# Kernel tuning notes

Measured on AMD Instinct MI355X. Metric: run time of the kernel, lower is better.

Reference implementation:

```python
import jax, jax.numpy as jnp
import numpy as np

B, D, L, H = 2, 64, 512, 1024  # batch, n_docs (timesteps), tokens per doc, bert hidden


def _ln(x, g, b):
    # torch.nn.LayerNorm over last dim, eps=1e-5
    m = jnp.mean(x, axis=-1, keepdims=True)
    v = jnp.mean((x - m) ** 2, axis=-1, keepdims=True)
    return (x - m) / jnp.sqrt(v + 1e-5) * g + b


def _ht(x):
    # Hardtanh(min=-8, max=8)
    return jnp.clip(x, -8.0, 8.0)


def setup_inputs() -> dict:
    key = jax.random.key(0)
    ks = jax.random.split(key, 12)
    xavier = lambda k, shape: jax.random.normal(k, shape, dtype=jnp.float32) * np.float32(np.sqrt(2.0 / sum(shape)))
    return {
        "trans": jax.random.normal(ks[0], (B, D, L, H), dtype=jnp.float32) * 0.1,  # frozen BERT last_hidden_state
        "document_mask": jax.random.bernoulli(ks[1], 0.9, (B, D)),
        "Wf": xavier(ks[2], (H, H)), "bf": jnp.ones((H,), jnp.float32),
        "Wi": xavier(ks[3], (H, H)), "bi": jnp.zeros((H,), jnp.float32),
        "Wg": xavier(ks[4], (H, H)), "bg": jnp.zeros((H,), jnp.float32),
        "Wo": xavier(ks[5], (H, H)), "bo": jnp.zeros((H,), jnp.float32),
        "Wp": xavier(ks[6], (H, H)), "bp": jnp.zeros((H,), jnp.float32),
        "tF": xavier(ks[7], (L,)), "tI": xavier(ks[8], (L,)), "tO": xavier(ks[9], (L,)),
        "c_gamma": jnp.ones((H,), jnp.float32), "c_beta": jnp.zeros((H,), jnp.float32),
        "h_gamma": jnp.ones((H,), jnp.float32), "h_beta": jnp.zeros((H,), jnp.float32),
    }


def _forward(trans, document_mask, Wf, bf, Wi, bi, Wg, bg, Wo, bo, Wp, bp,
             tF, tI, tO, c_gamma, c_beta, h_gamma, h_beta):
    b, d, l, h = trans.shape
    # docFlat @ transform: contract the token (l) axis -> [b, d, h]
    pF = jnp.einsum('bdlh,l->bdh', trans, tF)
    pI = jnp.einsum('bdlh,l->bdh', trans, tI)
    pO = jnp.einsum('bdlh,l->bdh', trans, tO)

    def step(carry, xs):
        c, hs = carry                      # each [b, h]
        pf, pi, po, m = xs                 # [b, h] x3, [b] bool
        nC = _ln(c, c_gamma, c_beta)
        nH = _ln(hs, h_gamma, h_beta)
        f = jax.nn.sigmoid(_ht(nH @ Wf.T + bf) + pf)
        c2 = c * f
        i = jax.nn.sigmoid(_ht(nH @ Wi.T + bi) + pi)
        g = _ht(jax.nn.gelu(nH @ Wg.T + bg, approximate=False) + pi)
        c2 = c2 + i * g
        o = jax.nn.sigmoid(_ht(nH @ Wo.T + bo) + po)
        h2 = o * _ht(jax.nn.gelu(nC @ Wp.T + bp, approximate=False))
        mm = m[:, None]
        h2 = jnp.where(mm, h2, hs)
        c2 = jnp.where(mm, c2, c)
        c2 = jnp.clip(c2, -10.0, 10.0)
        h2 = jnp.clip(h2, -10.0, 10.0)
        return (c2, h2), None

    init = (jnp.zeros((b, h), trans.dtype), jnp.zeros((b, h), trans.dtype))
    xs = (pF.transpose(1, 0, 2), pI.transpose(1, 0, 2), pO.transpose(1, 0, 2), document_mask.T)
    (c_fin, h_fin), _ = jax.lax.scan(step, init, xs)
    return h_fin  # [b, h] (original returns [b, h, 1])


def reference(trans, document_mask, Wf, bf, Wi, bi, Wg, bg, Wo, bo, Wp, bp,
              tF, tI, tO, c_gamma, c_beta, h_gamma, h_beta):
    return _forward(trans, document_mask, Wf, bf, Wi, bi, Wg, bg, Wo, bo, Wp, bp,
                    tF, tI, tO, c_gamma, c_beta, h_gamma, h_beta)
```

## Files before the change

kernel.cpp:

```cpp
#include <hip/hip_runtime.h>
#include <math.h>


#define NBLK 256

__device__ __forceinline__ float sigf(float x)   { return 1.0f / (1.0f + __expf(-x)); }
__device__ __forceinline__ float geluf(float x)  { return 0.5f * x * (1.0f + erff(x * 0.70710678118654752f)); }
__device__ __forceinline__ float clampf(float x, float lo, float hi) { return fminf(fmaxf(x, lo), hi); }

__device__ __forceinline__ void astf(float* p, float v) {
    __hip_atomic_store(p, v, __ATOMIC_RELAXED, __HIP_MEMORY_SCOPE_AGENT);
}
__device__ __forceinline__ float aldf(const float* p) {
    return __hip_atomic_load(p, __ATOMIC_RELAXED, __HIP_MEMORY_SCOPE_AGENT);
}
__device__ __forceinline__ void astu(unsigned* p, unsigned v) {
    __hip_atomic_store(p, v, __ATOMIC_RELAXED, __HIP_MEMORY_SCOPE_AGENT);
}
__device__ __forceinline__ unsigned aldu(const unsigned* p) {
    return __hip_atomic_load(p, __ATOMIC_RELAXED, __HIP_MEMORY_SCOPE_AGENT);
}

__global__ __launch_bounds__(256, 1) void fused_kernel(
    const float* __restrict__ trans, const int* __restrict__ mask,
    const float* __restrict__ Wf, const float* __restrict__ bf,
    const float* __restrict__ Wi, const float* __restrict__ bi,
    const float* __restrict__ Wg, const float* __restrict__ bg,
    const float* __restrict__ Wo, const float* __restrict__ bo,
    const float* __restrict__ Wp, const float* __restrict__ bp,
    const float* __restrict__ tF, const float* __restrict__ tI, const float* __restrict__ tO,
    const float* __restrict__ c_gamma, const float* __restrict__ c_beta,
    const float* __restrict__ h_gamma, const float* __restrict__ h_beta,
    float* __restrict__ ws, float* __restrict__ out)
{
    const int t    = threadIdx.x;
    const int lane = t & 63;
    const int wv   = t >> 6;
    const int blk  = blockIdx.x;
    const int hrow = (blk << 2) + wv;

    unsigned* flags = (unsigned*)ws;
    unsigned* rel   = flags + 256;
    float* stC = ws + 512;
    float* stH = ws + 4608;
    float* pF  = ws + 8704;
    float* pI  = pF + 131072;
    float* pO  = pI + 131072;

    __shared__ float smem[2][4][1024];

    float4 wfr[4], wir[4], wgr[4], wor[4], wpr[4];
    {
        const float4* rf = (const float4*)(Wf + (size_t)hrow * 1024);
        const float4* ri = (const float4*)(Wi + (size_t)hrow * 1024);
        const float4* rg = (const float4*)(Wg + (size_t)hrow * 1024);
        const float4* ro = (const float4*)(Wo + (size_t)hrow * 1024);
        const float4* rp = (const float4*)(Wp + (size_t)hrow * 1024);
        #pragma unroll
        for (int q = 0; q < 4; ++q) {
            const int k4 = lane + 64 * q;
            wfr[q] = rf[k4]; wir[q] = ri[k4]; wgr[q] = rg[k4];
            wor[q] = ro[k4]; wpr[q] = rp[k4];
        }
    }
    const float bfv = bf[hrow], biv = bi[hrow], bgv = bg[hrow], bov = bo[hrow], bpv = bp[hrow];

    {
        float* sF = &smem[0][0][0];
        float* sI = &smem[0][0][512];
        float* sO = &smem[0][1][0];
        sF[t] = tF[t]; sF[t + 256] = tF[t + 256];
        sI[t] = tI[t]; sI[t + 256] = tI[t + 256];
        sO[t] = tO[t]; sO[t + 256] = tO[t + 256];
        __syncthreads();

        const int bd = blk >> 1;
        const int h0 = (blk & 1) * 512;
        const int s  = t & 127;
        const int g  = t >> 7;
        const float4* tr = (const float4*)trans + (size_t)bd * 512 * 256 + (h0 >> 2) + s;

        float4 aF = make_float4(0.f,0.f,0.f,0.f);
        float4 aI = make_float4(0.f,0.f,0.f,0.f);
        float4 aO = make_float4(0.f,0.f,0.f,0.f);
        #pragma unroll 8
        for (int li = 0; li < 256; ++li) {
            const int l = g + 2 * li;
            float4 v = tr[(size_t)l * 256];
            const float wf = sF[l], wi = sI[l], wo = sO[l];
            aF.x = fmaf(v.x, wf, aF.x); aF.y = fmaf(v.y, wf, aF.y);
            aF.z = fmaf(v.z, wf, aF.z); aF.w = fmaf(v.w, wf, aF.w);
            aI.x = fmaf(v.x, wi, aI.x); aI.y = fmaf(v.y, wi, aI.y);
            aI.z = fmaf(v.z, wi, aI.z); aI.w = fmaf(v.w, wi, aI.w);
            aO.x = fmaf(v.x, wo, aO.x); aO.y = fmaf(v.y, wo, aO.y);
            aO.z = fmaf(v.z, wo, aO.z); aO.w = fmaf(v.w, wo, aO.w);
        }
        float4* cmb = (float4*)&smem[0][2][0];
        if (g == 1) { cmb[s] = aF; cmb[128 + s] = aI; cmb[256 + s] = aO; }
        __syncthreads();
        if (g == 0) {
            const float4 bF = cmb[s], bI = cmb[128 + s], bO = cmb[256 + s];
            aF.x += bF.x; aF.y += bF.y; aF.z += bF.z; aF.w += bF.w;
            aI.x += bI.x; aI.y += bI.y; aI.z += bI.z; aI.w += bI.w;
            aO.x += bO.x; aO.y += bO.y; aO.z += bO.z; aO.w += bO.w;
            const int base = bd * 1024 + h0 + 4 * s;
            astf(&pF[base+0], aF.x); astf(&pF[base+1], aF.y);
            astf(&pF[base+2], aF.z); astf(&pF[base+3], aF.w);
            astf(&pI[base+0], aI.x); astf(&pI[base+1], aI.y);
            astf(&pI[base+2], aI.z); astf(&pI[base+3], aI.w);
            astf(&pO[base+0], aO.x); astf(&pO[base+1], aO.y);
            astf(&pO[base+2], aO.z); astf(&pO[base+3], aO.w);
        }
    }
    __syncthreads();
    if (t == 0) astu(&flags[blk], 1u);

    float sfv, siv, sgv, sov, spv, bfb, bib, bgb, bob, bpb;
    {
        float4 gh4[4], bh4[4], gc4[4], bc4[4];
        const float4* Gh = (const float4*)h_gamma;
        const float4* Bh = (const float4*)h_beta;
        const float4* Gc = (const float4*)c_gamma;
        const float4* Bc = (const float4*)c_beta;
        #pragma unroll
        for (int q = 0; q < 4; ++q) {
            const int k4 = lane + 64 * q;
            gh4[q] = Gh[k4]; bh4[q] = Bh[k4]; gc4[q] = Gc[k4]; bc4[q] = Bc[k4];
        }
        bfb = bib = bgb = bob = bpb = 0.f;
        #pragma unroll
        for (int q = 0; q < 4; ++q) {
            bfb += wfr[q].x*bh4[q].x + wfr[q].y*bh4[q].y + wfr[q].z*bh4[q].z + wfr[q].w*bh4[q].w;
            bib += wir[q].x*bh4[q].x + wir[q].y*bh4[q].y + wir[q].z*bh4[q].z + wir[q].w*bh4[q].w;
            bgb += wgr[q].x*bh4[q].x + wgr[q].y*bh4[q].y + wgr[q].z*bh4[q].z + wgr[q].w*bh4[q].w;
            bob += wor[q].x*bh4[q].x + wor[q].y*bh4[q].y + wor[q].z*bh4[q].z + wor[q].w*bh4[q].w;
            bpb += wpr[q].x*bc4[q].x + wpr[q].y*bc4[q].y + wpr[q].z*bc4[q].z + wpr[q].w*bc4[q].w;
        }
        #pragma unroll
        for (int q = 0; q < 4; ++q) {
            wfr[q].x *= gh4[q].x; wfr[q].y *= gh4[q].y; wfr[q].z *= gh4[q].z; wfr[q].w *= gh4[q].w;
            wir[q].x *= gh4[q].x; wir[q].y *= gh4[q].y; wir[q].z *= gh4[q].z; wir[q].w *= gh4[q].w;
            wgr[q].x *= gh4[q].x; wgr[q].y *= gh4[q].y; wgr[q].z *= gh4[q].z; wgr[q].w *= gh4[q].w;
            wor[q].x *= gh4[q].x; wor[q].y *= gh4[q].y; wor[q].z *= gh4[q].z; wor[q].w *= gh4[q].w;
            wpr[q].x *= gc4[q].x; wpr[q].y *= gc4[q].y; wpr[q].z *= gc4[q].z; wpr[q].w *= gc4[q].w;
        }
        sfv = siv = sgv = sov = spv = 0.f;
        #pragma unroll
        for (int q = 0; q < 4; ++q) {
            sfv += wfr[q].x + wfr[q].y + wfr[q].z + wfr[q].w;
            siv += wir[q].x + wir[q].y + wir[q].z + wir[q].w;
            sgv += wgr[q].x + wgr[q].y + wgr[q].z + wgr[q].w;
            sov += wor[q].x + wor[q].y + wor[q].z + wor[q].w;
            spv += wpr[q].x + wpr[q].y + wpr[q].z + wpr[q].w;
        }
        #pragma unroll
        for (int off = 32; off; off >>= 1) {
            sfv += __shfl_xor(sfv, off); siv += __shfl_xor(siv, off);
            sgv += __shfl_xor(sgv, off); sov += __shfl_xor(sov, off);
            spv += __shfl_xor(spv, off);
            bfb += __shfl_xor(bfb, off); bib += __shfl_xor(bib, off);
            bgb += __shfl_xor(bgb, off); bob += __shfl_xor(bob, off);
            bpb += __shfl_xor(bpb, off);
        }
    }

    if (blk == 0) {
        if (wv == 0) {
            for (;;) {
                const unsigned a0 = aldu(&flags[lane]);
                const unsigned a1 = aldu(&flags[lane + 64]);
                const unsigned a2 = aldu(&flags[lane + 128]);
                const unsigned a3 = aldu(&flags[lane + 192]);
                const int ok = (a0 >= 1u) && (a1 >= 1u) && (a2 >= 1u) && (a3 >= 1u);
                if (__all(ok)) break;
                __builtin_amdgcn_s_sleep(1);
            }
            if (lane < 16) astu(&rel[lane * 16], 1u);
        }
    } else if (t == 0) {
        while (aldu(&rel[(blk & 15) * 16]) < 1u) __builtin_amdgcn_s_sleep(2);
    }
    __syncthreads();

    float c_prev = 0.f, h_prev = 0.f;

    for (int d = 0; d < 64; ++d) {
        const int par = d & 1;
        const float* cc = stC + par * 2048;
        const float* hc = stH + par * 2048;
        float* cn = stC + (par ^ 1) * 2048;
        float* hn = stH + (par ^ 1) * 2048;
        float (*sm)[1024] = smem[par];

        float pfv = 0.f, piv = 0.f, pov = 0.f;
        int mv = 1;
        if (lane < 2) {
            const int pidx = (lane * 64 + d) * 1024 + hrow;
            pfv = aldf(&pF[pidx]); piv = aldf(&pI[pidx]); pov = aldf(&pO[pidx]);
            mv = mask[lane * 64 + d];
        }

        {
            const unsigned tgt = (unsigned)(d + 1);
            if (blk == 0) {
                if (wv == 0) {
                    for (;;) {
                        const unsigned a0 = aldu(&flags[lane]);
                        const unsigned a1 = aldu(&flags[lane + 64]);
                        const unsigned a2 = aldu(&flags[lane + 128]);
                        const unsigned a3 = aldu(&flags[lane + 192]);
                        const int ok = (a0 >= tgt) && (a1 >= tgt) && (a2 >= tgt) && (a3 >= tgt);
                        if (__all(ok)) break;
                        __builtin_amdgcn_s_sleep(1);
                    }
                    if (lane < 16) astu(&rel[lane * 16], tgt);
                }
            } else if (t == 0) {
                while (aldu(&rel[(blk & 15) * 16]) < tgt) __builtin_amdgcn_s_sleep(2);
            }
            __syncthreads();
        }

        float lh0[4], lh1[4], lc0[4], lc1[4];
        #pragma unroll
        for (int j = 0; j < 4; ++j) {
            const int e = t + 256 * j;
            lh0[j] = aldf(hc + e);        lh1[j] = aldf(hc + 1024 + e);
            lc0[j] = aldf(cc + e);        lc1[j] = aldf(cc + 1024 + e);
        }
        #pragma unroll
        for (int j = 0; j < 4; ++j) {
            const int e = t + 256 * j;
            sm[0][e] = lh0[j]; sm[1][e] = lh1[j];
            sm[2][e] = lc0[j]; sm[3][e] = lc1[j];
        }
        __syncthreads();

        float zf0=0,zf1=0,zi0=0,zi1=0,zg0=0,zg1=0,zo0=0,zo1=0,zp0=0,zp1=0;
        float sH0=0,qH0=0,sH1=0,qH1=0,sC0=0,qC0=0,sC1=0,qC1=0;
        #pragma unroll
        for (int q = 0; q < 4; ++q) {
            const int k4 = lane + 64 * q;
            const float4 n0 = ((const float4*)sm[0])[k4];
            const float4 n1 = ((const float4*)sm[1])[k4];
            const float4 m0 = ((const float4*)sm[2])[k4];
            const float4 m1 = ((const float4*)sm[3])[k4];
            zf0 += wfr[q].x*n0.x + wfr[q].y*n0.y + wfr[q].z*n0.z + wfr[q].w*n0.w;
            zf1 += wfr[q].x*n1.x + wfr[q].y*n1.y + wfr[q].z*n1.z + wfr[q].w*n1.w;
            zi0 += wir[q].x*n0.x + wir[q].y*n0.y + wir[q].z*n0.z + wir[q].w*n0.w;
            zi1 += wir[q].x*n1.x + wir[q].y*n1.y + wir[q].z*n1.z + wir[q].w*n1.w;
            zg0 += wgr[q].x*n0.x + wgr[q].y*n0.y + wgr[q].z*n0.z + wgr[q].w*n0.w;
            zg1 += wgr[q].x*n1.x + wgr[q].y*n1.y + wgr[q].z*n1.z + wgr[q].w*n1.w;
            zo0 += wor[q].x*n0.x + wor[q].y*n0.y + wor[q].z*n0.z + wor[q].w*n0.w;
            zo1 += wor[q].x*n1.x + wor[q].y*n1.y + wor[q].z*n1.z + wor[q].w*n1.w;
            zp0 += wpr[q].x*m0.x + wpr[q].y*m0.y + wpr[q].z*m0.z + wpr[q].w*m0.w;
            zp1 += wpr[q].x*m1.x + wpr[q].y*m1.y + wpr[q].z*m1.z + wpr[q].w*m1.w;
            sH0 += n0.x + n0.y + n0.z + n0.w;
            qH0 += n0.x*n0.x + n0.y*n0.y + n0.z*n0.z + n0.w*n0.w;
            sH1 += n1.x + n1.y + n1.z + n1.w;
            qH1 += n1.x*n1.x + n1.y*n1.y + n1.z*n1.z + n1.w*n1.w;
            sC0 += m0.x + m0.y + m0.z + m0.w;
            qC0 += m0.x*m0.x + m0.y*m0.y + m0.z*m0.z + m0.w*m0.w;
            sC1 += m1.x + m1.y + m1.z + m1.w;
            qC1 += m1.x*m1.x + m1.y*m1.y + m1.z*m1.z + m1.w*m1.w;
        }
        #pragma unroll
        for (int off = 32; off; off >>= 1) {
            zf0 += __shfl_xor(zf0, off); zf1 += __shfl_xor(zf1, off);
            zi0 += __shfl_xor(zi0, off); zi1 += __shfl_xor(zi1, off);
            zg0 += __shfl_xor(zg0, off); zg1 += __shfl_xor(zg1, off);
            zo0 += __shfl_xor(zo0, off); zo1 += __shfl_xor(zo1, off);
            zp0 += __shfl_xor(zp0, off); zp1 += __shfl_xor(zp1, off);
            sH0 += __shfl_xor(sH0, off); qH0 += __shfl_xor(qH0, off);
            sH1 += __shfl_xor(sH1, off); qH1 += __shfl_xor(qH1, off);
            sC0 += __shfl_xor(sC0, off); qC0 += __shfl_xor(qC0, off);
            sC1 += __shfl_xor(sC1, off); qC1 += __shfl_xor(qC1, off);
        }

        if (lane < 2) {
            const int b = lane;
            const float inv = 1.0f / 1024.0f;
            const float mh = (b ? sH1 : sH0) * inv;
            const float qh = (b ? qH1 : qH0) * inv;
            const float rh = rsqrtf(qh - mh * mh + 1e-5f);
            const float mc = (b ? sC1 : sC0) * inv;
            const float qc = (b ? qC1 : qC0) * inv;
            const float rc = rsqrtf(qc - mc * mc + 1e-5f);
            const float zf = rh * ((b ? zf1 : zf0) - mh * sfv) + bfb;
            const float zi = rh * ((b ? zi1 : zi0) - mh * siv) + bib;
            const float zg = rh * ((b ? zg1 : zg0) - mh * sgv) + bgb;
            const float zo = rh * ((b ? zo1 : zo0) - mh * sov) + bob;
            const float zp = rc * ((b ? zp1 : zp0) - mc * spv) + bpb;
            const float f  = sigf(clampf(zf + bfv, -8.f, 8.f) + pfv);
            const float ig = sigf(clampf(zi + biv, -8.f, 8.f) + piv);
            const float g  = clampf(geluf(zg + bgv) + piv, -8.f, 8.f);
            const float o  = sigf(clampf(zo + bov, -8.f, 8.f) + pov);
            const float hp = clampf(geluf(zp + bpv), -8.f, 8.f);
            float c2 = c_prev * f + ig * g;
            float h2 = o * hp;
            if (mv == 0) { c2 = c_prev; h2 = h_prev; }
            c2 = clampf(c2, -10.f, 10.f);
            h2 = clampf(h2, -10.f, 10.f);
            c_prev = c2; h_prev = h2;
            if (d == 63) {
                out[b * 1024 + hrow] = h2;
            } else {
                astf(cn + b * 1024 + hrow, c2);
                astf(hn + b * 1024 + hrow, h2);
            }
        }

        if (d == 63) break;
        __syncthreads();
        if (t == 0) astu(&flags[blk], (unsigned)(d + 2));
    }
}

extern "C" void kernel_launch(void* const* d_in, const int* in_sizes, int n_in,
                              void* d_out, int out_size, void* d_ws, size_t ws_size,
                              hipStream_t stream)
{
    const float* trans = (const float*)d_in[0];
    const int*   mask  = (const int*)d_in[1];
    const float* Wf = (const float*)d_in[2];  const float* bf = (const float*)d_in[3];
    const float* Wi = (const float*)d_in[4];  const float* bi = (const float*)d_in[5];
    const float* Wg = (const float*)d_in[6];  const float* bg = (const float*)d_in[7];
    const float* Wo = (const float*)d_in[8];  const float* bo = (const float*)d_in[9];
    const float* Wp = (const float*)d_in[10]; const float* bp = (const float*)d_in[11];
    const float* tF = (const float*)d_in[12];
    const float* tI = (const float*)d_in[13];
    const float* tO = (const float*)d_in[14];
    const float* c_gamma = (const float*)d_in[15];
    const float* c_beta  = (const float*)d_in[16];
    const float* h_gamma = (const float*)d_in[17];
    const float* h_beta  = (const float*)d_in[18];

    float* ws  = (float*)d_ws;
    float* out = (float*)d_out;

    hipMemsetAsync(d_ws, 0, 8704u * sizeof(float), stream);

    void* args[] = { (void*)&trans, (void*)&mask,
                     (void*)&Wf, (void*)&bf, (void*)&Wi, (void*)&bi,
                     (void*)&Wg, (void*)&bg, (void*)&Wo, (void*)&bo,
                     (void*)&Wp, (void*)&bp,
                     (void*)&tF, (void*)&tI, (void*)&tO,
                     (void*)&c_gamma, (void*)&c_beta, (void*)&h_gamma, (void*)&h_beta,
                     (void*)&ws, (void*)&out };
    hipLaunchCooperativeKernel((void*)fused_kernel, dim3(256), dim3(256), args, 0, stream);
}
```

Baseline: 801.9 us.

## Concentrate recurrence on 64 blocks of 1024 threads with flat flag polling

Launches 1024-thread blocks and assigns 16 hidden rows per block, so the sequential recurrence runs on only 64 active blocks while all 256 blocks still do the token-reduction prologue with an extra tree-reduction stage. The hierarchical release barrier driven by block 0 is replaced by each active block polling the 64 flags directly. The aim is to cut per-step grid-synchronisation latency across the 64 timesteps. The cost is more prologue work per block, more register pressure at 1024 threads, and more polling traffic on the flag array.

```diff
diff --git a/kernel.cpp b/kernel.cpp
--- a/kernel.cpp
+++ b/kernel.cpp
@@ -2,7 +2,7 @@
 #include <math.h>
 
 
-#define NBLK 256
+#define NACT 64
 
 __device__ __forceinline__ float sigf(float x)   { return 1.0f / (1.0f + __expf(-x)); }
 __device__ __forceinline__ float geluf(float x)  { return 0.5f * x * (1.0f + erff(x * 0.70710678118654752f)); }
@@ -21,7 +21,7 @@
     return __hip_atomic_load(p, __ATOMIC_RELAXED, __HIP_MEMORY_SCOPE_AGENT);
 }
 
-__global__ __launch_bounds__(256, 1) void fused_kernel(
+__global__ __launch_bounds__(1024, 1) void fused_kernel(
     const float* __restrict__ trans, const int* __restrict__ mask,
     const float* __restrict__ Wf, const float* __restrict__ bf,
     const float* __restrict__ Wi, const float* __restrict__ bi,
@@ -37,20 +37,26 @@
     const int lane = t & 63;
     const int wv   = t >> 6;
     const int blk  = blockIdx.x;
-    const int hrow = (blk << 2) + wv;
+    const bool act = (blk < NACT);
+    const int hrow = (blk << 4) + wv;
 
     unsigned* flags = (unsigned*)ws;
-    unsigned* rel   = flags + 256;
-    float* stC = ws + 512;
-    float* stH = ws + 4608;
-    float* pF  = ws + 8704;
+    float* stC = ws + 320;
+    float* stH = ws + 4416;
+    float* pF  = ws + 8512;
     float* pI  = pF + 131072;
     float* pO  = pI + 131072;
 
     __shared__ float smem[2][4][1024];
+    float* sbase = &smem[0][0][0];
+    float4* cmb4 = (float4*)sbase;
+    float* sF = sbase + 6144;
+    float* sI = sbase + 6656;
+    float* sO = sbase + 7168;
 
     float4 wfr[4], wir[4], wgr[4], wor[4], wpr[4];
-    {
+    float bfv = 0.f, biv = 0.f, bgv = 0.f, bov = 0.f, bpv = 0.f;
+    if (act) {
         const float4* rf = (const float4*)(Wf + (size_t)hrow * 1024);
         const float4* ri = (const float4*)(Wi + (size_t)hrow * 1024);
         const float4* rg = (const float4*)(Wg + (size_t)hrow * 1024);
@@ -62,16 +68,11 @@
             wfr[q] = rf[k4]; wir[q] = ri[k4]; wgr[q] = rg[k4];
             wor[q] = ro[k4]; wpr[q] = rp[k4];
         }
-    }
-    const float bfv = bf[hrow], biv = bi[hrow], bgv = bg[hrow], bov = bo[hrow], bpv = bp[hrow];
+        bfv = bf[hrow]; biv = bi[hrow]; bgv = bg[hrow]; bov = bo[hrow]; bpv = bp[hrow];
+    }
 
     {
-        float* sF = &smem[0][0][0];
-        float* sI = &smem[0][0][512];
-        float* sO = &smem[0][1][0];
-        sF[t] = tF[t]; sF[t + 256] = tF[t + 256];
-        sI[t] = tI[t]; sI[t + 256] = tI[t + 256];
-        sO[t] = tO[t]; sO[t + 256] = tO[t + 256];
+        if (t < 512) { sF[t] = tF[t]; sI[t] = tI[t]; sO[t] = tO[t]; }
         __syncthreads();
 
         const int bd = blk >> 1;
@@ -84,8 +85,8 @@
         float4 aI = make_float4(0.f,0.f,0.f,0.f);
         float4 aO = make_float4(0.f,0.f,0.f,0.f);
         #pragma unroll 8
-        for (int li = 0; li < 256; ++li) {
-            const int l = g + 2 * li;
+        for (int li = 0; li < 64; ++li) {
+            const int l = g + 8 * li;
             float4 v = tr[(size_t)l * 256];
             const float wf = sF[l], wi = sI[l], wo = sO[l];
             aF.x = fmaf(v.x, wf, aF.x); aF.y = fmaf(v.y, wf, aF.y);
@@ -95,14 +96,39 @@
             aO.x = fmaf(v.x, wo, aO.x); aO.y = fmaf(v.y, wo, aO.y);
             aO.z = fmaf(v.z, wo, aO.z); aO.w = fmaf(v.w, wo, aO.w);
         }
-        float4* cmb = (float4*)&smem[0][2][0];
-        if (g == 1) { cmb[s] = aF; cmb[128 + s] = aI; cmb[256 + s] = aO; }
-        __syncthreads();
-        if (g == 0) {
-            const float4 bF = cmb[s], bI = cmb[128 + s], bO = cmb[256 + s];
+        if (g >= 4) {
+            const int gp = g - 4;
+            cmb4[(gp * 3 + 0) * 128 + s] = aF;
+            cmb4[(gp * 3 + 1) * 128 + s] = aI;
+            cmb4[(gp * 3 + 2) * 128 + s] = aO;
+        }
+        __syncthreads();
+        if (g < 4) {
+            const float4 bF = cmb4[(g * 3 + 0) * 128 + s];
+            const float4 bI = cmb4[(g * 3 + 1) * 128 + s];
+            const float4 bO = cmb4[(g * 3 + 2) * 128 + s];
             aF.x += bF.x; aF.y += bF.y; aF.z += bF.z; aF.w += bF.w;
             aI.x += bI.x; aI.y += bI.y; aI.z += bI.z; aI.w += bI.w;
             aO.x += bO.x; aO.y += bO.y; aO.z += bO.z; aO.w += bO.w;
+        }
+        __syncthreads();
+        if (g >= 1 && g < 4) {
+            const int gp = g - 1;
+            cmb4[(gp * 3 + 0) * 128 + s] = aF;
+            cmb4[(gp * 3 + 1) * 128 + s] = aI;
+            cmb4[(gp * 3 + 2) * 128 + s] = aO;
+        }
+        __syncthreads();
+        if (g == 0) {
+            #pragma unroll
+            for (int gp = 0; gp < 3; ++gp) {
+                const float4 bF = cmb4[(gp * 3 + 0) * 128 + s];
+                const float4 bI = cmb4[(gp * 3 + 1) * 128 + s];
+                const float4 bO = cmb4[(gp * 3 + 2) * 128 + s];
+                aF.x += bF.x; aF.y += bF.y; aF.z += bF.z; aF.w += bF.w;
+                aI.x += bI.x; aI.y += bI.y; aI.z += bI.z; aI.w += bI.w;
+                aO.x += bO.x; aO.y += bO.y; aO.z += bO.z; aO.w += bO.w;
+            }
             const int base = bd * 1024 + h0 + 4 * s;
             astf(&pF[base+0], aF.x); astf(&pF[base+1], aF.y);
             astf(&pF[base+2], aF.z); astf(&pF[base+3], aF.w);
@@ -114,6 +140,7 @@
     }
     __syncthreads();
     if (t == 0) astu(&flags[blk], 1u);
+    if (!act) return;
 
     float sfv, siv, sgv, sov, spv, bfb, bib, bgb, bob, bpb;
     {
@@ -164,21 +191,16 @@
         }
     }
 
-    if (blk == 0) {
-        if (wv == 0) {
-            for (;;) {
-                const unsigned a0 = aldu(&flags[lane]);
-                const unsigned a1 = aldu(&flags[lane + 64]);
-                const unsigned a2 = aldu(&flags[lane + 128]);
-                const unsigned a3 = aldu(&flags[lane + 192]);
-                const int ok = (a0 >= 1u) && (a1 >= 1u) && (a2 >= 1u) && (a3 >= 1u);
-                if (__all(ok)) break;
-                __builtin_amdgcn_s_sleep(1);
-            }
-            if (lane < 16) astu(&rel[lane * 16], 1u);
-        }
-    } else if (t == 0) {
-        while (aldu(&rel[(blk & 15) * 16]) < 1u) __builtin_amdgcn_s_sleep(2);
+    if (wv == 0) {
+        for (;;) {
+            const unsigned a0 = aldu(&flags[lane]);
+            const unsigned a1 = aldu(&flags[lane + 64]);
+            const unsigned a2 = aldu(&flags[lane + 128]);
+            const unsigned a3 = aldu(&flags[lane + 192]);
+            const int ok = (a0 >= 1u) && (a1 >= 1u) && (a2 >= 1u) && (a3 >= 1u);
+            if (__all(ok)) break;
+            __builtin_amdgcn_s_sleep(1);
+        }
     }
     __syncthreads();
 
@@ -200,40 +222,21 @@
             mv = mask[lane * 64 + d];
         }
 
-        {
+        if (wv == 0) {
             const unsigned tgt = (unsigned)(d + 1);
-            if (blk == 0) {
-                if (wv == 0) {
-                    for (;;) {
-                        const unsigned a0 = aldu(&flags[lane]);
-                        const unsigned a1 = aldu(&flags[lane + 64]);
-                        const unsigned a2 = aldu(&flags[lane + 128]);
-                        const unsigned a3 = aldu(&flags[lane + 192]);
-                        const int ok = (a0 >= tgt) && (a1 >= tgt) && (a2 >= tgt) && (a3 >= tgt);
-                        if (__all(ok)) break;
-                        __builtin_amdgcn_s_sleep(1);
-                    }
-                    if (lane < 16) astu(&rel[lane * 16], tgt);
-                }
-            } else if (t == 0) {
-                while (aldu(&rel[(blk & 15) * 16]) < tgt) __builtin_amdgcn_s_sleep(2);
+            for (;;) {
+                const unsigned a0 = aldu(&flags[lane]);
+                if (__all(a0 >= tgt)) break;
+                __builtin_amdgcn_s_sleep(1);
             }
-            __syncthreads();
-        }
-
-        float lh0[4], lh1[4], lc0[4], lc1[4];
-        #pragma unroll
-        for (int j = 0; j < 4; ++j) {
-            const int e = t + 256 * j;
-            lh0[j] = aldf(hc + e);        lh1[j] = aldf(hc + 1024 + e);
-            lc0[j] = aldf(cc + e);        lc1[j] = aldf(cc + 1024 + e);
-        }
-        #pragma unroll
-        for (int j = 0; j < 4; ++j) {
-            const int e = t + 256 * j;
-            sm[0][e] = lh0[j]; sm[1][e] = lh1[j];
-            sm[2][e] = lc0[j]; sm[3][e] = lc1[j];
-        }
+        }
+        __syncthreads();
+
+        const float lh0 = aldf(hc + t);
+        const float lh1 = aldf(hc + 1024 + t);
+        const float lc0 = aldf(cc + t);
+        const float lc1 = aldf(cc + 1024 + t);
+        sm[0][t] = lh0; sm[1][t] = lh1; sm[2][t] = lc0; sm[3][t] = lc1;
         __syncthreads();
 
         float zf0=0,zf1=0,zi0=0,zi1=0,zg0=0,zg1=0,zo0=0,zo1=0,zp0=0,zp1=0;
@@ -338,7 +341,7 @@
     float* ws  = (float*)d_ws;
     float* out = (float*)d_out;
 
-    hipMemsetAsync(d_ws, 0, 8704u * sizeof(float), stream);
+    hipMemsetAsync(d_ws, 0, 8512u * sizeof(float), stream);
 
     void* args[] = { (void*)&trans, (void*)&mask,
                      (void*)&Wf, (void*)&bf, (void*)&Wi, (void*)&bi,
@@ -347,5 +350,5 @@
                      (void*)&tF, (void*)&tI, (void*)&tO,
                      (void*)&c_gamma, (void*)&c_beta, (void*)&h_gamma, (void*)&h_beta,
                      (void*)&ws, (void*)&out };
-    hipLaunchCooperativeKernel((void*)fused_kernel, dim3(256), dim3(256), args, 0, stream);
-}
+    hipLaunchCooperativeKernel((void*)fused_kernel, dim3(256), dim3(1024), args, 0, stream);
+}
```

Result: slower. 1.276 ms (+59.1%).
